# Kernel optimization log

Hardware: AMD Instinct MI355X
Metric: run time of the kernel (lower is better)

## Reference

```python
import jax, jax.numpy as jnp
import numpy as np

N = 100000
K = 8
DK = 16          # d_in/K == d_out/K
E = 1600000
EPS = 1e-12      # torch F.normalize eps


def setup_inputs() -> dict:
    key = jax.random.key(0)
    k1, k2, k3, k4 = jax.random.split(key, 4)
    f_in = jax.random.normal(k1, (N, K, DK), dtype=jnp.float32)
    Ep = jax.random.randint(k2, (E, 2), 0, N, dtype=jnp.int64)
    En = jax.random.randint(k3, (E, 2), 0, N, dtype=jnp.int64)
    # xavier_uniform over (K, 5*DK, DK): fan_in=5*DK, fan_out=DK
    limit = float(np.sqrt(6.0 / (5 * DK + DK)))
    W = jax.random.uniform(k4, (K, 5 * DK, DK), dtype=jnp.float32,
                           minval=-limit, maxval=limit)
    b = jnp.zeros((1, K, DK), dtype=jnp.float32)
    return {"f_in": f_in, "Ep": Ep, "En": En, "W": W, "b": b}


def _aggregate(Ep, En, f_in):
    n = f_in.shape[0]
    seg = lambda vals, idx: jax.ops.segment_sum(vals, idx, num_segments=n)
    m_p_out = seg(f_in[Ep[:, 1]], Ep[:, 0])
    m_p_in = seg(f_in[Ep[:, 0]], Ep[:, 1])
    m_n_out = seg(f_in[En[:, 1]], En[:, 0])
    m_n_in = seg(f_in[En[:, 0]], En[:, 1])
    return m_p_out, m_p_in, m_n_out, m_n_in


def reference(f_in, Ep, En, W, b):
    m_p_out, m_p_in, m_n_out, m_n_in = _aggregate(Ep, En, f_in)
    # (N, K, 5*DK)
    m_concat = jnp.concatenate([m_p_out, m_p_in, f_in, m_n_out, m_n_in], axis=2)
    # per-factor grouped matmul: (N,K,5DK) x (K,5DK,DK) -> (N,K,DK)
    f_out = jnp.einsum('nkf,kfo->nko', m_concat, W) + b
    a = jnp.tanh(f_out)
    # F.normalize: L2 over dim=1 (factor axis), clamp_min eps
    norm = jnp.maximum(jnp.linalg.norm(a, axis=1, keepdims=True), EPS)
    return a / norm
```

## Files before the change

kernel.cpp:

```cpp
#include <hip/hip_runtime.h>
#include <math.h>


#define ROW 128
#define ROW4 32
#define BC   256
#define BSH  8
#define WNUM 512

__device__ __forceinline__ void push_entry(
    int* __restrict__ cnt, int* __restrict__ ovfCnt, int* __restrict__ ovf,
    int* __restrict__ idxbuf, int seg, int src, int PAD, int ovfCap)
{
    int slot = atomicAdd(&cnt[seg], 1);
    if (slot < PAD) {
        idxbuf[(size_t)seg * PAD + slot] = src;
    } else {
        int oi = atomicAdd(ovfCnt, 1);
        if (oi < ovfCap) { ovf[2*oi] = seg; ovf[2*oi+1] = src; }
    }
}

__global__ __launch_bounds__(256) void fill_kernel(
    const int4* __restrict__ Ep2, const int4* __restrict__ En2,
    const int* __restrict__ Ep, const int* __restrict__ En,
    int* __restrict__ cnt, int* __restrict__ ovfCnt, int* __restrict__ ovf,
    int* __restrict__ idxbuf, int Epairs, int Etail, int N, int PAD, int ovfCap)
{
    int i = blockIdx.x * 256 + threadIdx.x;
    int stride = gridDim.x * 256;
    for (int e = i; e < Epairs; e += stride) {
        int4 p = Ep2[e];
        push_entry(cnt, ovfCnt, ovf, idxbuf, 4*p.x + 0, p.y, PAD, ovfCap);
        push_entry(cnt, ovfCnt, ovf, idxbuf, 4*p.y + 1, p.x, PAD, ovfCap);
        push_entry(cnt, ovfCnt, ovf, idxbuf, 4*p.z + 0, p.w, PAD, ovfCap);
        push_entry(cnt, ovfCnt, ovf, idxbuf, 4*p.w + 1, p.z, PAD, ovfCap);
        int4 q = En2[e];
        push_entry(cnt, ovfCnt, ovf, idxbuf, 4*q.x + 2, q.y, PAD, ovfCap);
        push_entry(cnt, ovfCnt, ovf, idxbuf, 4*q.y + 3, q.x, PAD, ovfCap);
        push_entry(cnt, ovfCnt, ovf, idxbuf, 4*q.z + 2, q.w, PAD, ovfCap);
        push_entry(cnt, ovfCnt, ovf, idxbuf, 4*q.w + 3, q.z, PAD, ovfCap);
    }
    if (i == 0 && Etail) {
        int e = 2 * Epairs;
        int a = Ep[2*e], b = Ep[2*e+1];
        push_entry(cnt, ovfCnt, ovf, idxbuf, 4*a + 0, b, PAD, ovfCap);
        push_entry(cnt, ovfCnt, ovf, idxbuf, 4*b + 1, a, PAD, ovfCap);
        int c = En[2*e], d = En[2*e+1];
        push_entry(cnt, ovfCnt, ovf, idxbuf, 4*c + 2, d, PAD, ovfCap);
        push_entry(cnt, ovfCnt, ovf, idxbuf, 4*d + 3, c, PAD, ovfCap);
    }
}

__global__ __launch_bounds__(256) void fill_bucket(
    const int4* __restrict__ Ep2, const int4* __restrict__ En2,
    const int* __restrict__ Ep, const int* __restrict__ En,
    int* __restrict__ cnt2, int* __restrict__ cells,
    int* __restrict__ ovfCnt, int* __restrict__ ovf,
    int Epairs, int Etail, int B, int CAP, int ovfCap)
{
    __shared__ int lcnt[1024];
    const int w = blockIdx.x;
    int* __restrict__ mycell = cells + (size_t)w * B * CAP;

    for (int i = threadIdx.x; i < 1024; i += 256) lcnt[i] = 0;
    __syncthreads();

    auto pushB = [&](int dst, int l, int src) {
        int bkt  = dst >> BSH;
        int slot = atomicAdd(&lcnt[bkt], 1);
        if (slot < CAP) {
            mycell[(size_t)bkt * CAP + slot] =
                src | ((dst & (BC - 1)) << 17) | (l << 25);
        } else {
            int oi = atomicAdd(ovfCnt, 1);
            if (oi < ovfCap) { ovf[2*oi] = 4*dst + l; ovf[2*oi+1] = src; }
        }
    };

    int stride = gridDim.x * 256;
    for (int e = blockIdx.x * 256 + threadIdx.x; e < Epairs; e += stride) {
        int4 p = Ep2[e];
        pushB(p.x, 0, p.y); pushB(p.y, 1, p.x);
        pushB(p.z, 0, p.w); pushB(p.w, 1, p.z);
        int4 q = En2[e];
        pushB(q.x, 2, q.y); pushB(q.y, 3, q.x);
        pushB(q.z, 2, q.w); pushB(q.w, 3, q.z);
    }
    if (w == 0 && threadIdx.x == 0 && Etail) {
        int e = 2 * Epairs;
        int a = Ep[2*e], b = Ep[2*e+1];
        pushB(a, 0, b); pushB(b, 1, a);
        int c = En[2*e], d = En[2*e+1];
        pushB(c, 2, d); pushB(d, 3, c);
    }
    __syncthreads();
    for (int b = threadIdx.x; b < B; b += 256) {
        int v = lcnt[b];
        cnt2[(size_t)w * B + b] = (v < CAP) ? v : CAP;
    }
}

__global__ __launch_bounds__(256) void build_csr(
    const int* __restrict__ cnt2, const int* __restrict__ cells,
    int* __restrict__ cnt, int* __restrict__ idxbuf,
    int* __restrict__ ovfCnt, int* __restrict__ ovf,
    int N, int B, int CAP, int PAD, int ovfCap)
{
    __shared__ int scnt[4 * BC];
    const int b = blockIdx.x;
    const int nodeBase = b << BSH;

    for (int i = threadIdx.x; i < 4 * BC; i += 256) scnt[i] = 0;
    __syncthreads();

    for (int w = threadIdx.x; w < WNUM; w += 256) {
        int c = cnt2[(size_t)w * B + b];
        const int* __restrict__ cell = cells + ((size_t)w * B + b) * CAP;
        for (int i = 0; i < c; ++i) {
            int p    = cell[i];
            int src  = p & 0x1FFFF;
            int dl   = (p >> 17) & (BC - 1);
            int l    = (p >> 25) & 3;
            int segl = (dl << 2) | l;
            int slot = atomicAdd(&scnt[segl], 1);
            if (slot < PAD) {
                idxbuf[(size_t)((nodeBase + dl) * 4 + l) * PAD + slot] = src;
            } else {
                int oi = atomicAdd(ovfCnt, 1);
                if (oi < ovfCap) {
                    ovf[2*oi] = (nodeBase + dl) * 4 + l; ovf[2*oi+1] = src;
                }
            }
        }
    }
    __syncthreads();
    for (int i = threadIdx.x; i < 4 * BC; i += 256) {
        int node = nodeBase + (i >> 2);
        if (node < N) cnt[node * 4 + (i & 3)] = scnt[i];
    }
}

__global__ __launch_bounds__(256) void ovf_kernel(
    const float* __restrict__ f_in, const float* __restrict__ W,
    const int* __restrict__ ovfCnt, const int* __restrict__ ovf,
    float* __restrict__ out, int N, int ovfCap)
{
    const int t = threadIdx.x & 127;
    const int k = t >> 4;
    const int o = t & 15;
    int nOv = *ovfCnt;
    if (nOv > ovfCap) nOv = ovfCap;
    const int group  = blockIdx.x * 2 + (threadIdx.x >> 7);
    const int stride = gridDim.x * 2;
    for (int i = group; i < nOv; i += stride) {
        int seg = ovf[2*i], src = ovf[2*i+1];
        int l = seg & 3;
        int dst = seg >> 2;
        int s = (l < 2) ? l : l + 1;
        float y = 0.f;
#pragma unroll
        for (int ii = 0; ii < 16; ++ii)
            y += f_in[(size_t)src*ROW + k*16 + ii] * W[k*1280 + (s*16 + ii)*16 + o];
        unsafeAtomicAdd(&out[(size_t)dst*ROW + t], y);
    }
}

__global__ __launch_bounds__(256, 4) void pull_kernel(
    const float4* __restrict__ f_in4,
    const float*  __restrict__ f_in,
    const int*    __restrict__ cnt,
    const int*    __restrict__ idxbuf,
    const float*  __restrict__ W,
    const float*  __restrict__ bias,
    float*        __restrict__ out,
    int N, int PAD)
{
    __shared__ float4 sacc4[2][5][ROW4];
    __shared__ float  syp[2][ROW];
    __shared__ float  sa[ROW];

    const int tid  = threadIdx.x;
    const int elem = tid & 127;
    const int h    = tid >> 7;
    const int k    = elem >> 4;
    const int o    = elem & 15;
    const int oct  = tid >> 5;
    const int l    = oct >> 1;
    const int hh   = oct & 1;
    const int e4   = tid & 31;
    const int slot = (l < 2) ? l : l + 1;

    float w[5][8];
#pragma unroll
    for (int s = 0; s < 5; ++s)
#pragma unroll
        for (int i = 0; i < 8; ++i)
            w[s][i] = W[k*1280 + (s*16 + h*8 + i)*16 + o];
    const float bb = bias[elem];

    for (int n = blockIdx.x; n < N; n += gridDim.x) {
        float pre = (h == 0) ? out[(size_t)n*ROW + elem] : 0.f;

        int c = cnt[4*n + l];
        if (c > PAD) c = PAD;
        const size_t base = (size_t)(4*n + l) * PAD;
        const int mid = (c + 1) >> 1;
        int j         = hh ? mid : 0;
        const int end = hh ? c   : mid;

        float4 acc = make_float4(0.f, 0.f, 0.f, 0.f);
        for (; j + 3 < end; j += 4) {
            int j0 = idxbuf[base + j],     j1 = idxbuf[base + j + 1];
            int j2 = idxbuf[base + j + 2], j3 = idxbuf[base + j + 3];
            float4 r0 = f_in4[(size_t)j0*ROW4 + e4];
            float4 r1 = f_in4[(size_t)j1*ROW4 + e4];
            float4 r2 = f_in4[(size_t)j2*ROW4 + e4];
            float4 r3 = f_in4[(size_t)j3*ROW4 + e4];
            acc.x += r0.x + r1.x + r2.x + r3.x;
            acc.y += r0.y + r1.y + r2.y + r3.y;
            acc.z += r0.z + r1.z + r2.z + r3.z;
            acc.w += r0.w + r1.w + r2.w + r3.w;
        }
        for (; j < end; ++j) {
            float4 r = f_in4[(size_t)idxbuf[base + j]*ROW4 + e4];
            acc.x += r.x; acc.y += r.y; acc.z += r.z; acc.w += r.w;
        }
        sacc4[hh][slot][e4] = acc;
        if (oct == 0) sacc4[0][2][e4] = f_in4[(size_t)n*ROW4 + e4];
        if (oct == 1) sacc4[1][2][e4] = make_float4(0.f, 0.f, 0.f, 0.f);
        __syncthreads();

        float y = 0.f;
#pragma unroll
        for (int s = 0; s < 5; ++s) {
            const float* m0 = (const float*)&sacc4[0][s][0] + k*16 + h*8;
            const float* m1 = (const float*)&sacc4[1][s][0] + k*16 + h*8;
#pragma unroll
            for (int i = 0; i < 8; ++i)
                y += (m0[i] + m1[i]) * w[s][i];
        }
        syp[h][elem] = y;
        __syncthreads();

        float a = 0.f;
        if (h == 0) {
            a = tanhf(syp[0][elem] + syp[1][elem] + bb + pre);
            sa[elem] = a;
        }
        __syncthreads();
        if (h == 0) {
            float ss = 0.f;
#pragma unroll
            for (int k2 = 0; k2 < 8; ++k2) {
                float v = sa[k2*16 + o];
                ss += v * v;
            }
            out[(size_t)n*ROW + elem] = a / fmaxf(sqrtf(ss), 1e-12f);
        }
        __syncthreads();
    }
}

extern "C" void kernel_launch(void* const* d_in, const int* in_sizes, int n_in,
                              void* d_out, int out_size, void* d_ws, size_t ws_size,
                              hipStream_t stream) {
    const float* f_in = (const float*)d_in[0];
    const int*   Ep   = (const int*)d_in[1];
    const int*   En   = (const int*)d_in[2];
    const float* W    = (const float*)d_in[3];
    const float* b    = (const float*)d_in[4];
    float* out = (float*)d_out;

    const int N = in_sizes[0] / ROW;
    const int E = in_sizes[1] / 2;
    const int Epairs = E / 2;
    const int Etail  = E & 1;
    const int M = 4 * N;
    const int B = (N + BC - 1) / BC;

    bool newpath = (N <= 131072) && (B <= 1024);
    int PAD = 0, CAP = 0;
    if (newpath) {
        const int cfgs[][2] = {{64,48},{56,48},{48,48},{48,40},{40,40},{40,32},
                               {32,32},{32,24},{24,24},{24,16},{16,16}};
        bool found = false;
        for (int i = 0; i < (int)(sizeof(cfgs)/sizeof(cfgs[0])); ++i) {
            int pad = cfgs[i][0], cap = cfgs[i][1];
            size_t need = ((size_t)M + 64 + (size_t)WNUM * B
                           + (size_t)M * pad
                           + (size_t)WNUM * B * cap) * sizeof(int)
                          + 512 * 1024;
            if (need <= ws_size) { PAD = pad; CAP = cap; found = true; break; }
        }
        if (!found) newpath = false;
    }

    if (newpath) {
        int* cnt    = (int*)d_ws;
        int* ovfCnt = cnt + M;
        int* cnt2   = ovfCnt + 64;
        int* idxbuf = cnt2 + (size_t)WNUM * B;
        int* cells  = idxbuf + (size_t)M * PAD;
        int* ovf    = cells + (size_t)WNUM * B * CAP;
        size_t used = ((size_t)M + 64 + (size_t)WNUM * B
                       + (size_t)M * PAD + (size_t)WNUM * B * CAP) * sizeof(int);
        size_t left = ws_size - used;
        size_t ovfCapSz = left / (2 * sizeof(int));
        int ovfCap = (int)(ovfCapSz > (size_t)(1 << 22) ? (1 << 22) : ovfCapSz);
        if (ovfCap < 1) ovfCap = 1;

        hipMemsetAsync(ovfCnt, 0, 64 * sizeof(int), stream);
        hipMemsetAsync(out, 0, (size_t)out_size * sizeof(float), stream);

        fill_bucket<<<WNUM, 256, 0, stream>>>((const int4*)Ep, (const int4*)En,
                                              Ep, En, cnt2, cells, ovfCnt, ovf,
                                              Epairs, Etail, B, CAP, ovfCap);
        build_csr<<<B, 256, 0, stream>>>(cnt2, cells, cnt, idxbuf,
                                         ovfCnt, ovf, N, B, CAP, PAD, ovfCap);
        ovf_kernel<<<256, 256, 0, stream>>>(f_in, W, ovfCnt, ovf, out, N, ovfCap);
        pull_kernel<<<8192, 256, 0, stream>>>((const float4*)f_in, f_in, cnt,
                                              idxbuf, W, b, out, N, PAD);
        return;
    }

    int PADf = 72;
    size_t fixed;
    do {
        PADf -= 8;
        fixed = ((size_t)M + 64 + (size_t)M * PADf) * sizeof(int);
    } while (PADf > 8 && fixed + 512 * 1024 > ws_size);
    size_t left = (ws_size > fixed) ? (ws_size - fixed) : 8;
    size_t ovfCapSz = left / (2 * sizeof(int));
    int ovfCap = (int)(ovfCapSz > (size_t)(1 << 22) ? (1 << 22) : ovfCapSz);
    if (ovfCap < 1) ovfCap = 1;

    int* cnt    = (int*)d_ws;
    int* ovfCnt = cnt + M;
    int* idxbuf = ovfCnt + 64;
    int* ovf    = idxbuf + (size_t)M * PADf;

    hipMemsetAsync(cnt, 0, ((size_t)M + 64) * sizeof(int), stream);
    hipMemsetAsync(out, 0, (size_t)out_size * sizeof(float), stream);

    fill_kernel<<<2048, 256, 0, stream>>>((const int4*)Ep, (const int4*)En,
                                          Ep, En, cnt, ovfCnt, ovf, idxbuf,
                                          Epairs, Etail, N, PADf, ovfCap);
    ovf_kernel<<<64, 256, 0, stream>>>(f_in, W, ovfCnt, ovf, out, N, ovfCap);
    pull_kernel<<<8192, 256, 0, stream>>>((const float4*)f_in, f_in, cnt,
                                          idxbuf, W, b, out, N, PADf);
}
```

Measured before the change: 794.6 us.

## Software-pipeline pull_kernel gathers with double-buffered shared memory; widen build_csr

pull_kernel now gathers neighbour rows for the next node into registers while the current node's grouped matmul, tanh and normalize run, using double-buffered shared accumulators and dropping one barrier per iteration. It also skips reading the prior output when no overflow entries exist, and raises the occupancy hint. build_csr moves to 512 threads per block and reads bucket cells as int4 vectors. The aim is to hide gather latency behind compute, at the cost of more registers and shared memory, and the int4 reads assume cell rows are 16-byte aligned.

```diff
diff --git a/kernel.cpp b/kernel.cpp
--- a/kernel.cpp
+++ b/kernel.cpp
@@ -101,7 +101,7 @@
     }
 }
 
-__global__ __launch_bounds__(256) void build_csr(
+__global__ __launch_bounds__(512) void build_csr(
     const int* __restrict__ cnt2, const int* __restrict__ cells,
     int* __restrict__ cnt, int* __restrict__ idxbuf,
     int* __restrict__ ovfCnt, int* __restrict__ ovf,
@@ -111,31 +111,39 @@
     const int b = blockIdx.x;
     const int nodeBase = b << BSH;
 
-    for (int i = threadIdx.x; i < 4 * BC; i += 256) scnt[i] = 0;
+    for (int i = threadIdx.x; i < 4 * BC; i += 512) scnt[i] = 0;
     __syncthreads();
 
-    for (int w = threadIdx.x; w < WNUM; w += 256) {
+    auto proc = [&](int p) {
+        int src  = p & 0x1FFFF;
+        int dl   = (p >> 17) & (BC - 1);
+        int l    = (p >> 25) & 3;
+        int segl = (dl << 2) | l;
+        int slot = atomicAdd(&scnt[segl], 1);
+        if (slot < PAD) {
+            idxbuf[(size_t)((nodeBase + dl) * 4 + l) * PAD + slot] = src;
+        } else {
+            int oi = atomicAdd(ovfCnt, 1);
+            if (oi < ovfCap) {
+                ovf[2*oi] = (nodeBase + dl) * 4 + l; ovf[2*oi+1] = src;
+            }
+        }
+    };
+
+    for (int w = threadIdx.x; w < WNUM; w += 512) {
         int c = cnt2[(size_t)w * B + b];
-        const int* __restrict__ cell = cells + ((size_t)w * B + b) * CAP;
-        for (int i = 0; i < c; ++i) {
-            int p    = cell[i];
-            int src  = p & 0x1FFFF;
-            int dl   = (p >> 17) & (BC - 1);
-            int l    = (p >> 25) & 3;
-            int segl = (dl << 2) | l;
-            int slot = atomicAdd(&scnt[segl], 1);
-            if (slot < PAD) {
-                idxbuf[(size_t)((nodeBase + dl) * 4 + l) * PAD + slot] = src;
-            } else {
-                int oi = atomicAdd(ovfCnt, 1);
-                if (oi < ovfCap) {
-                    ovf[2*oi] = (nodeBase + dl) * 4 + l; ovf[2*oi+1] = src;
-                }
-            }
+        const int4* __restrict__ cell4 =
+            (const int4*)(cells + ((size_t)w * B + b) * CAP);
+        for (int i = 0; i < c; i += 4) {
+            int4 v = cell4[i >> 2];
+            proc(v.x);
+            if (i + 1 < c) proc(v.y);
+            if (i + 2 < c) proc(v.z);
+            if (i + 3 < c) proc(v.w);
         }
     }
     __syncthreads();
-    for (int i = threadIdx.x; i < 4 * BC; i += 256) {
+    for (int i = threadIdx.x; i < 4 * BC; i += 512) {
         int node = nodeBase + (i >> 2);
         if (node < N) cnt[node * 4 + (i & 3)] = scnt[i];
     }
@@ -166,17 +174,18 @@
     }
 }
 
-__global__ __launch_bounds__(256, 4) void pull_kernel(
+__global__ __launch_bounds__(256, 6) void pull_kernel(
     const float4* __restrict__ f_in4,
     const float*  __restrict__ f_in,
     const int*    __restrict__ cnt,
     const int*    __restrict__ idxbuf,
     const float*  __restrict__ W,
     const float*  __restrict__ bias,
+    const int*    __restrict__ ovfCnt,
     float*        __restrict__ out,
     int N, int PAD)
 {
-    __shared__ float4 sacc4[2][5][ROW4];
+    __shared__ float4 sacc4[2][2][5][ROW4];
     __shared__ float  syp[2][ROW];
     __shared__ float  sa[ROW];
 
@@ -198,17 +207,20 @@
         for (int i = 0; i < 8; ++i)
             w[s][i] = W[k*1280 + (s*16 + h*8 + i)*16 + o];
     const float bb = bias[elem];
-
-    for (int n = blockIdx.x; n < N; n += gridDim.x) {
-        float pre = (h == 0) ? out[(size_t)n*ROW + elem] : 0.f;
-
-        int c = cnt[4*n + l];
+    const int haveOvf = *ovfCnt;
+
+    const int stride = gridDim.x;
+
+    float4 racc  = make_float4(0.f, 0.f, 0.f, 0.f);
+    float4 rself = make_float4(0.f, 0.f, 0.f, 0.f);
+
+    auto do_gather = [&](int node) {
+        int c = cnt[4*node + l];
         if (c > PAD) c = PAD;
-        const size_t base = (size_t)(4*n + l) * PAD;
+        const size_t base = (size_t)(4*node + l) * PAD;
         const int mid = (c + 1) >> 1;
         int j         = hh ? mid : 0;
         const int end = hh ? c   : mid;
-
         float4 acc = make_float4(0.f, 0.f, 0.f, 0.f);
         for (; j + 3 < end; j += 4) {
             int j0 = idxbuf[base + j],     j1 = idxbuf[base + j + 1];
@@ -226,16 +238,34 @@
             float4 r = f_in4[(size_t)idxbuf[base + j]*ROW4 + e4];
             acc.x += r.x; acc.y += r.y; acc.z += r.z; acc.w += r.w;
         }
-        sacc4[hh][slot][e4] = acc;
-        if (oct == 0) sacc4[0][2][e4] = f_in4[(size_t)n*ROW4 + e4];
-        if (oct == 1) sacc4[1][2][e4] = make_float4(0.f, 0.f, 0.f, 0.f);
+        racc = acc;
+        if (oct == 0) rself = f_in4[(size_t)node*ROW4 + e4];
+    };
+
+    if (oct == 1) {
+        sacc4[0][1][2][e4] = make_float4(0.f, 0.f, 0.f, 0.f);
+        sacc4[1][1][2][e4] = make_float4(0.f, 0.f, 0.f, 0.f);
+    }
+
+    int n = blockIdx.x;
+    if (n < N) do_gather(n);
+    int cur = 0;
+
+    for (; n < N; n += stride) {
+        sacc4[cur][hh][slot][e4] = racc;
+        if (oct == 0) sacc4[cur][0][2][e4] = rself;
+        float pre = 0.f;
+        if (h == 0 && haveOvf) pre = out[(size_t)n*ROW + elem];
         __syncthreads();
 
+        int nn = n + stride;
+        if (nn < N) do_gather(nn);
+
         float y = 0.f;
 #pragma unroll
         for (int s = 0; s < 5; ++s) {
-            const float* m0 = (const float*)&sacc4[0][s][0] + k*16 + h*8;
-            const float* m1 = (const float*)&sacc4[1][s][0] + k*16 + h*8;
+            const float* m0 = (const float*)&sacc4[cur][0][s][0] + k*16 + h*8;
+            const float* m1 = (const float*)&sacc4[cur][1][s][0] + k*16 + h*8;
 #pragma unroll
             for (int i = 0; i < 8; ++i)
                 y += (m0[i] + m1[i]) * w[s][i];
@@ -243,12 +273,12 @@
         syp[h][elem] = y;
         __syncthreads();
 
-        float a = 0.f;
         if (h == 0) {
-            a = tanhf(syp[0][elem] + syp[1][elem] + bb + pre);
+            float a = tanhf(syp[0][elem] + syp[1][elem] + bb + pre);
             sa[elem] = a;
         }
         __syncthreads();
+
         if (h == 0) {
             float ss = 0.f;
 #pragma unroll
@@ -256,9 +286,9 @@
                 float v = sa[k2*16 + o];
                 ss += v * v;
             }
-            out[(size_t)n*ROW + elem] = a / fmaxf(sqrtf(ss), 1e-12f);
-        }
-        __syncthreads();
+            out[(size_t)n*ROW + elem] = sa[elem] / fmaxf(sqrtf(ss), 1e-12f);
+        }
+        cur ^= 1;
     }
 }
 
@@ -316,11 +346,11 @@
         fill_bucket<<<WNUM, 256, 0, stream>>>((const int4*)Ep, (const int4*)En,
                                               Ep, En, cnt2, cells, ovfCnt, ovf,
                                               Epairs, Etail, B, CAP, ovfCap);
-        build_csr<<<B, 256, 0, stream>>>(cnt2, cells, cnt, idxbuf,
+        build_csr<<<B, 512, 0, stream>>>(cnt2, cells, cnt, idxbuf,
                                          ovfCnt, ovf, N, B, CAP, PAD, ovfCap);
         ovf_kernel<<<256, 256, 0, stream>>>(f_in, W, ovfCnt, ovf, out, N, ovfCap);
         pull_kernel<<<8192, 256, 0, stream>>>((const float4*)f_in, f_in, cnt,
-                                              idxbuf, W, b, out, N, PAD);
+                                              idxbuf, W, b, ovfCnt, out, N, PAD);
         return;
     }
 
@@ -348,5 +378,5 @@
                                           Epairs, Etail, N, PADf, ovfCap);
     ovf_kernel<<<64, 256, 0, stream>>>(f_in, W, ovfCnt, ovf, out, N, ovfCap);
     pull_kernel<<<8192, 256, 0, stream>>>((const float4*)f_in, f_in, cnt,
-                                          idxbuf, W, b, out, N, PADf);
-}
+                                          idxbuf, W, b, ovfCnt, out, N, PADf);
+}
```

Result: slower. 985.1 us (+24.0%).

## Split CSR build into two halves per bucket with more bucket-fill blocks

Applied to the files above, without the earlier changes.

The CSR build now runs two 512-thread blocks per node bucket. Each block fills its own half of every segment's padded index list and writes a separate count, so the pull kernel reads two independent halves. The fill stage can use 1024 bucket writers, cell entries are read as int4, and the pull kernel skips reading the output accumulator when no overflow occurred. The cost is more workspace for counts and a smaller per-half capacity, which can push more edges onto the slower overflow path when degrees are uneven.

```diff
diff --git a/kernel.cpp b/kernel.cpp
--- a/kernel.cpp
+++ b/kernel.cpp
@@ -6,7 +6,6 @@
 #define ROW4 32
 #define BC   256
 #define BSH  8
-#define WNUM 512
 
 __device__ __forceinline__ void push_entry(
     int* __restrict__ cnt, int* __restrict__ ovfCnt, int* __restrict__ ovf,
@@ -101,43 +100,55 @@
     }
 }
 
-__global__ __launch_bounds__(256) void build_csr(
+__global__ __launch_bounds__(512) void build_csr(
     const int* __restrict__ cnt2, const int* __restrict__ cells,
     int* __restrict__ cnt, int* __restrict__ idxbuf,
     int* __restrict__ ovfCnt, int* __restrict__ ovf,
-    int N, int B, int CAP, int PAD, int ovfCap)
+    int N, int B, int CAP, int PAD, int wn, int ovfCap)
 {
     __shared__ int scnt[4 * BC];
-    const int b = blockIdx.x;
+    const int b     = blockIdx.x >> 1;
+    const int hf    = blockIdx.x & 1;
+    const int HP    = PAD >> 1;
+    const int halfW = wn >> 1;
     const int nodeBase = b << BSH;
 
-    for (int i = threadIdx.x; i < 4 * BC; i += 256) scnt[i] = 0;
+    for (int i = threadIdx.x; i < 4 * BC; i += 512) scnt[i] = 0;
     __syncthreads();
 
-    for (int w = threadIdx.x; w < WNUM; w += 256) {
+    auto proc = [&](int p) {
+        int src  = p & 0x1FFFF;
+        int dl   = (p >> 17) & (BC - 1);
+        int l    = (p >> 25) & 3;
+        int segl = (dl << 2) | l;
+        int slot = atomicAdd(&scnt[segl], 1);
+        int seg  = (nodeBase + dl) * 4 + l;
+        if (slot < HP) {
+            idxbuf[(size_t)seg * PAD + hf * HP + slot] = src;
+        } else {
+            int oi = atomicAdd(ovfCnt, 1);
+            if (oi < ovfCap) { ovf[2*oi] = seg; ovf[2*oi+1] = src; }
+        }
+    };
+
+    const int wEnd = (hf + 1) * halfW;
+    for (int w = hf * halfW + threadIdx.x; w < wEnd; w += 512) {
         int c = cnt2[(size_t)w * B + b];
-        const int* __restrict__ cell = cells + ((size_t)w * B + b) * CAP;
-        for (int i = 0; i < c; ++i) {
-            int p    = cell[i];
-            int src  = p & 0x1FFFF;
-            int dl   = (p >> 17) & (BC - 1);
-            int l    = (p >> 25) & 3;
-            int segl = (dl << 2) | l;
-            int slot = atomicAdd(&scnt[segl], 1);
-            if (slot < PAD) {
-                idxbuf[(size_t)((nodeBase + dl) * 4 + l) * PAD + slot] = src;
-            } else {
-                int oi = atomicAdd(ovfCnt, 1);
-                if (oi < ovfCap) {
-                    ovf[2*oi] = (nodeBase + dl) * 4 + l; ovf[2*oi+1] = src;
-                }
-            }
+        const int4* __restrict__ cell4 =
+            (const int4*)(cells + ((size_t)w * B + b) * CAP);
+        for (int i = 0; i < c; i += 4) {
+            int4 v = cell4[i >> 2];
+            proc(v.x);
+            if (i + 1 < c) proc(v.y);
+            if (i + 2 < c) proc(v.z);
+            if (i + 3 < c) proc(v.w);
         }
     }
     __syncthreads();
-    for (int i = threadIdx.x; i < 4 * BC; i += 256) {
+    for (int i = threadIdx.x; i < 4 * BC; i += 512) {
         int node = nodeBase + (i >> 2);
-        if (node < N) cnt[node * 4 + (i & 3)] = scnt[i];
+        if (node < N)
+            cnt[(((size_t)node * 4 + (i & 3)) << 1) + hf] = scnt[i];
     }
 }
 
@@ -173,8 +184,9 @@
     const int*    __restrict__ idxbuf,
     const float*  __restrict__ W,
     const float*  __restrict__ bias,
+    const int*    __restrict__ ovfCnt,
     float*        __restrict__ out,
-    int N, int PAD)
+    int N, int PAD, int SPLIT)
 {
     __shared__ float4 sacc4[2][5][ROW4];
     __shared__ float  syp[2][ROW];
@@ -190,6 +202,7 @@
     const int hh   = oct & 1;
     const int e4   = tid & 31;
     const int slot = (l < 2) ? l : l + 1;
+    const int HP   = PAD >> 1;
 
     float w[5][8];
 #pragma unroll
@@ -198,16 +211,26 @@
         for (int i = 0; i < 8; ++i)
             w[s][i] = W[k*1280 + (s*16 + h*8 + i)*16 + o];
     const float bb = bias[elem];
+    const int haveOvf = *ovfCnt;
 
     for (int n = blockIdx.x; n < N; n += gridDim.x) {
-        float pre = (h == 0) ? out[(size_t)n*ROW + elem] : 0.f;
-
-        int c = cnt[4*n + l];
-        if (c > PAD) c = PAD;
-        const size_t base = (size_t)(4*n + l) * PAD;
-        const int mid = (c + 1) >> 1;
-        int j         = hh ? mid : 0;
-        const int end = hh ? c   : mid;
+        float pre = (h == 0 && haveOvf) ? out[(size_t)n*ROW + elem] : 0.f;
+
+        int j, end;
+        size_t base;
+        if (SPLIT) {
+            int c = cnt[(((size_t)4*n + l) << 1) + hh];
+            if (c > HP) c = HP;
+            base = (size_t)(4*n + l) * PAD + (size_t)hh * HP;
+            j = 0; end = c;
+        } else {
+            int c = cnt[4*n + l];
+            if (c > PAD) c = PAD;
+            base = (size_t)(4*n + l) * PAD;
+            int mid = (c + 1) >> 1;
+            j   = hh ? mid : 0;
+            end = hh ? c   : mid;
+        }
 
         float4 acc = make_float4(0.f, 0.f, 0.f, 0.f);
         for (; j + 3 < end; j += 4) {
@@ -280,31 +303,39 @@
     const int B = (N + BC - 1) / BC;
 
     bool newpath = (N <= 131072) && (B <= 1024);
-    int PAD = 0, CAP = 0;
+    int PAD = 0, CAP = 0, WN = 0;
     if (newpath) {
-        const int cfgs[][2] = {{64,48},{56,48},{48,48},{48,40},{40,40},{40,32},
-                               {32,32},{32,24},{24,24},{24,16},{16,16}};
-        bool found = false;
-        for (int i = 0; i < (int)(sizeof(cfgs)/sizeof(cfgs[0])); ++i) {
-            int pad = cfgs[i][0], cap = cfgs[i][1];
-            size_t need = ((size_t)M + 64 + (size_t)WNUM * B
-                           + (size_t)M * pad
-                           + (size_t)WNUM * B * cap) * sizeof(int)
-                          + 512 * 1024;
-            if (need <= ws_size) { PAD = pad; CAP = cap; found = true; break; }
-        }
-        if (!found) newpath = false;
+        const int cfg1k[][2] = {{64,48},{48,40},{48,32},{40,32},{40,24},
+                                {32,24},{32,16},{24,16},{16,16}};
+        const int cfg512[][2] = {{64,48},{56,48},{48,48},{48,40},{40,40},
+                                 {40,32},{32,32},{32,24},{24,24},{24,16},
+                                 {16,16}};
+        const int wnl[2] = {1024, 512};
+        for (int wi = 0; wi < 2 && !WN; ++wi) {
+            int wn = wnl[wi];
+            const int (*cfg)[2] = wi ? cfg512 : cfg1k;
+            int ncfg = wi ? 11 : 9;
+            for (int i = 0; i < ncfg; ++i) {
+                int pad = cfg[i][0], cap = cfg[i][1];
+                size_t need = ((size_t)2*M + 64 + (size_t)wn * B
+                               + (size_t)M * pad
+                               + (size_t)wn * B * cap) * sizeof(int)
+                              + 512 * 1024;
+                if (need <= ws_size) { PAD = pad; CAP = cap; WN = wn; break; }
+            }
+        }
+        if (!WN) newpath = false;
     }
 
     if (newpath) {
         int* cnt    = (int*)d_ws;
-        int* ovfCnt = cnt + M;
+        int* ovfCnt = cnt + (size_t)2*M;
         int* cnt2   = ovfCnt + 64;
-        int* idxbuf = cnt2 + (size_t)WNUM * B;
+        int* idxbuf = cnt2 + (size_t)WN * B;
         int* cells  = idxbuf + (size_t)M * PAD;
-        int* ovf    = cells + (size_t)WNUM * B * CAP;
-        size_t used = ((size_t)M + 64 + (size_t)WNUM * B
-                       + (size_t)M * PAD + (size_t)WNUM * B * CAP) * sizeof(int);
+        int* ovf    = cells + (size_t)WN * B * CAP;
+        size_t used = ((size_t)2*M + 64 + (size_t)WN * B
+                       + (size_t)M * PAD + (size_t)WN * B * CAP) * sizeof(int);
         size_t left = ws_size - used;
         size_t ovfCapSz = left / (2 * sizeof(int));
         int ovfCap = (int)(ovfCapSz > (size_t)(1 << 22) ? (1 << 22) : ovfCapSz);
@@ -313,14 +344,16 @@
         hipMemsetAsync(ovfCnt, 0, 64 * sizeof(int), stream);
         hipMemsetAsync(out, 0, (size_t)out_size * sizeof(float), stream);
 
-        fill_bucket<<<WNUM, 256, 0, stream>>>((const int4*)Ep, (const int4*)En,
-                                              Ep, En, cnt2, cells, ovfCnt, ovf,
-                                              Epairs, Etail, B, CAP, ovfCap);
-        build_csr<<<B, 256, 0, stream>>>(cnt2, cells, cnt, idxbuf,
-                                         ovfCnt, ovf, N, B, CAP, PAD, ovfCap);
+        fill_bucket<<<WN, 256, 0, stream>>>((const int4*)Ep, (const int4*)En,
+                                            Ep, En, cnt2, cells, ovfCnt, ovf,
+                                            Epairs, Etail, B, CAP, ovfCap);
+        build_csr<<<2*B, 512, 0, stream>>>(cnt2, cells, cnt, idxbuf,
+                                           ovfCnt, ovf, N, B, CAP, PAD, WN,
+                                           ovfCap);
         ovf_kernel<<<256, 256, 0, stream>>>(f_in, W, ovfCnt, ovf, out, N, ovfCap);
         pull_kernel<<<8192, 256, 0, stream>>>((const float4*)f_in, f_in, cnt,
-                                              idxbuf, W, b, out, N, PAD);
+                                              idxbuf, W, b, ovfCnt, out, N,
+                                              PAD, 1);
         return;
     }
 
@@ -348,5 +381,6 @@
                                           Epairs, Etail, N, PADf, ovfCap);
     ovf_kernel<<<64, 256, 0, stream>>>(f_in, W, ovfCnt, ovf, out, N, ovfCap);
     pull_kernel<<<8192, 256, 0, stream>>>((const float4*)f_in, f_in, cnt,
-                                          idxbuf, W, b, out, N, PADf);
-}
+                                          idxbuf, W, b, ovfCnt, out, N,
+                                          PADf, 0);
+}
```

After: 814.1 us. 1.02x slower.
